# Kernel tuning notes

Hardware: AMD Instinct MI355X
Metric: run time of the kernel (lower is better)

The kernel has to match this reference:

```python
import jax, jax.numpy as jnp
import numpy as np

EMBED = 512
QDIM = 512
VDIM = 512
SRC = 4096
BSZ = 64


def setup_inputs() -> dict:
    key = jax.random.key(0)
    ks = jax.random.split(key, 6)
    query = jax.random.normal(ks[0], (BSZ, QDIM), dtype=jnp.float32)
    value = jax.random.normal(ks[1], (SRC, BSZ, VDIM), dtype=jnp.float32)
    key_padding_mask = jnp.zeros((SRC, BSZ), dtype=bool)
    # params: torch init uniform(-0.1, 0.1); b=0, g=sqrt(1/embed)
    Wq = jax.random.uniform(ks[2], (EMBED, QDIM), minval=-0.1, maxval=0.1, dtype=jnp.float32)
    Wv = jax.random.uniform(ks[3], (EMBED, VDIM), minval=-0.1, maxval=0.1, dtype=jnp.float32)
    v = jax.random.uniform(ks[4], (EMBED,), minval=-0.1, maxval=0.1, dtype=jnp.float32)
    b = jnp.zeros((EMBED,), dtype=jnp.float32)
    g = jnp.full((1,), np.sqrt(1.0 / EMBED), dtype=jnp.float32)
    return {"query": query, "value": value, "key_padding_mask": key_padding_mask,
            "Wq": Wq, "Wv": Wv, "v": v, "b": b, "g": g}


def reference(query, value, key_padding_mask, Wq, Wv, v, b, g):
    # projected_query: [1, bsz, embed]; key: [src, bsz, embed]
    pq = (query @ Wq.T)[None, :, :]
    key = jnp.einsum('sbv,ev->sbe', value, Wv)
    normed_v = g * v / jnp.linalg.norm(v)  # [embed]
    # attn_scores: [src, bsz]
    attn_scores = jnp.einsum('e,sbe->sb', normed_v, jnp.tanh(pq + key + b))
    attn_scores = jnp.where(key_padding_mask, -jnp.inf, attn_scores)
    attn_scores = jax.nn.softmax(attn_scores, axis=0)
    # context: [bsz, value_dim]
    context = jnp.einsum('sb,sbv->bv', attn_scores, value)
    return (context, attn_scores, attn_scores)
```

## Files before the change

### kernel.cpp

```cpp
#include <hip/hip_runtime.h>
#include <hip/hip_bf16.h>
#include <math.h>

typedef __bf16 bf16x8 __attribute__((ext_vector_type(8)));
typedef float  f32x4  __attribute__((ext_vector_type(4)));

#define SRC 4096
#define BSZ 64
#define EMB 512

__global__ void prep_all(const float* __restrict__ query, const float* __restrict__ Wq,
                         const float* __restrict__ bias, const float* __restrict__ v,
                         const float* __restrict__ g, const float* __restrict__ Wv,
                         float* __restrict__ nv, float* __restrict__ pqb,
                         __bf16* __restrict__ wvpk) {
  __shared__ float sh[EMB];
  __shared__ float red[256];
  const int blk = blockIdx.x, t = threadIdx.x;
  if (blk == 0) {
    float a = v[t], b = v[t + 256];
    red[t] = a * a + b * b;
    __syncthreads();
    for (int o = 128; o > 0; o >>= 1) {
      if (t < o) red[t] += red[t + o];
      __syncthreads();
    }
    float scale = g[0] / sqrtf(red[0]);
    nv[t]       = a * scale;
    nv[t + 256] = b * scale;
  } else if (blk <= 128) {
    int tid  = (blk - 1) * 256 + t;
    int lane = tid & 63;
    int ks   = (tid >> 6) & 15;
    int nsub = tid >> 10;
    int e  = nsub * 16 + (lane & 15);
    int k0 = ks * 32 + (lane >> 4) * 8;
    const float* src = Wv + (size_t)e * EMB + k0;
    bf16x8 o;
#pragma unroll
    for (int j = 0; j < 8; ++j) o[j] = (__bf16)src[j];
    *reinterpret_cast<bf16x8*>(wvpk + (size_t)tid * 8) = o;
  } else {
    int bb = blk - 129;
    int b = bb >> 1;
    int e = (bb & 1) * 256 + t;
    sh[t]       = query[b * EMB + t];
    sh[t + 256] = query[b * EMB + t + 256];
    __syncthreads();
    const float* wr = Wq + (size_t)e * EMB;
    float a0 = 0.f, a1 = 0.f;
#pragma unroll 8
    for (int k = 0; k < EMB; k += 8) {
      float4 q0 = *reinterpret_cast<const float4*>(&sh[k]);
      float4 w0 = *reinterpret_cast<const float4*>(&wr[k]);
      float4 q1 = *reinterpret_cast<const float4*>(&sh[k + 4]);
      float4 w1 = *reinterpret_cast<const float4*>(&wr[k + 4]);
      a0 += q0.x * w0.x + q0.y * w0.y + q0.z * w0.z + q0.w * w0.w;
      a1 += q1.x * w1.x + q1.y * w1.y + q1.z * w1.z + q1.w * w1.w;
    }
    pqb[b * EMB + e] = a0 + a1 + bias[e];
  }
}

__global__ __launch_bounds__(512, 4)
void scores_kernel(const float* __restrict__ value, const float* __restrict__ pqb,
                   const float* __restrict__ nv, const __bf16* __restrict__ wvpk,
                   float* __restrict__ scoresT) {
  __shared__ __bf16 As[BSZ * EMB];
  __shared__ float red[8][BSZ];
  const int s = blockIdx.x;
  const int t = threadIdx.x;

  {
    const int row = t >> 3, sub = t & 7;
    const float* src = value + (size_t)s * (BSZ * EMB) + (size_t)row * EMB + sub * 8;
#pragma unroll
    for (int j = 0; j < 8; ++j) {
      float4 v0 = *reinterpret_cast<const float4*>(src + j * 64);
      float4 v1 = *reinterpret_cast<const float4*>(src + j * 64 + 4);
      int kgp = (sub + j * 8) ^ (row & 7);
      bf16x8 o;
      o[0] = (__bf16)v0.x; o[1] = (__bf16)v0.y; o[2] = (__bf16)v0.z; o[3] = (__bf16)v0.w;
      o[4] = (__bf16)v1.x; o[5] = (__bf16)v1.y; o[6] = (__bf16)v1.z; o[7] = (__bf16)v1.w;
      *reinterpret_cast<bf16x8*>(&As[row * EMB + kgp * 8]) = o;
    }
  }
  __syncthreads();

  const int w = t >> 6, l = t & 63, lr = l & 15, lk = l >> 4;

  f32x4 acc[4][4];
#pragma unroll
  for (int m = 0; m < 4; ++m)
#pragma unroll
    for (int n = 0; n < 4; ++n)
#pragma unroll
      for (int r = 0; r < 4; ++r) acc[m][n][r] = 0.f;

  const __bf16* bp = wvpk + (size_t)(w * 4) * 16 * 512 + (size_t)l * 8;
  bf16x8 bq[2][4];
#pragma unroll
  for (int n = 0; n < 4; ++n)
    bq[0][n] = *reinterpret_cast<const bf16x8*>(bp + (size_t)(n * 16) * 512);

#pragma unroll
  for (int ksg = 0; ksg < 16; ++ksg) {
    if (ksg < 15) {
#pragma unroll
      for (int n = 0; n < 4; ++n)
        bq[(ksg + 1) & 1][n] =
            *reinterpret_cast<const bf16x8*>(bp + (size_t)(n * 16 + ksg + 1) * 512);
    }
    const int kgp = ((ksg * 4 + lk) ^ (lr & 7)) * 8;
#pragma unroll
    for (int m = 0; m < 4; ++m) {
      bf16x8 a = *reinterpret_cast<const bf16x8*>(&As[(m * 16 + lr) * EMB + kgp]);
#pragma unroll
      for (int n = 0; n < 4; ++n)
        acc[m][n] = __builtin_amdgcn_mfma_f32_16x16x32_bf16(a, bq[ksg & 1][n], acc[m][n], 0, 0, 0);
    }
  }

  float sc[16];
#pragma unroll
  for (int i = 0; i < 16; ++i) sc[i] = 0.f;
#pragma unroll
  for (int n = 0; n < 4; ++n) {
    int col = w * 64 + n * 16 + lr;
    float nvc = nv[col];
#pragma unroll
    for (int m = 0; m < 4; ++m) {
#pragma unroll
      for (int r = 0; r < 4; ++r) {
        int brow = m * 16 + lk * 4 + r;
        float x = acc[m][n][r] + pqb[brow * EMB + col];
        float e = __expf(2.0f * x);
        float rcp = __builtin_amdgcn_rcpf(1.0f + e);
        sc[m * 4 + r] += fmaf(-2.0f * nvc, rcp, nvc);
      }
    }
  }

#pragma unroll
  for (int i = 0; i < 16; ++i) {
    float vsum = sc[i];
#pragma unroll
    for (int off = 1; off < 16; off <<= 1) vsum += __shfl_xor(vsum, off, 64);
    if (lr == 0) red[w][(i >> 2) * 16 + lk * 4 + (i & 3)] = vsum;
  }
  __syncthreads();
  if (t < BSZ) {
    float total = 0.f;
#pragma unroll
    for (int ww = 0; ww < 8; ++ww) total += red[ww][t];
    scoresT[(size_t)t * SRC + s] = total;
  }
}

__global__ void softmax_k(const float* __restrict__ scoresT, const unsigned char* __restrict__ mask,
                          float* __restrict__ pT, float* __restrict__ attn0,
                          float* __restrict__ attn1) {
  __shared__ float buf[SRC];
  __shared__ float red[256];
  int b = blockIdx.x, t = threadIdx.x;
  float sum = 0.f;
  for (int s = t; s < SRC; s += 256) {
    float x = scoresT[(size_t)b * SRC + s];
    float e = mask[(size_t)s * BSZ + b] ? 0.f : __expf(x);
    buf[s] = e;
    sum += e;
  }
  red[t] = sum; __syncthreads();
  for (int o = 128; o > 0; o >>= 1) { if (t < o) red[t] += red[t + o]; __syncthreads(); }
  float inv = 1.0f / red[0];
  for (int s = t; s < SRC; s += 256) {
    float p = buf[s] * inv;
    pT[(size_t)b * SRC + s] = p;
    attn0[(size_t)s * BSZ + b] = p;
    attn1[(size_t)s * BSZ + b] = p;
  }
}

__global__ __launch_bounds__(256)
void ctx_partial(const float* __restrict__ value, const float* __restrict__ pT,
                 float* __restrict__ parts) {
  int blk = blockIdx.x;
  int c = blk >> 6;
  int b = blk & 63;
  int t = threadIdx.x;
  int f4 = t & 127, half = t >> 7;
  const float* pb = pT + (size_t)b * SRC + c * 256 + half;
  const float* vb = value + ((size_t)(c * 256 + half) * BSZ + b) * EMB + f4 * 4;
  float4 acc = make_float4(0.f, 0.f, 0.f, 0.f);
#pragma unroll 8
  for (int j = 0; j < 128; ++j) {
    float p = pb[j * 2];
    float4 vv = *reinterpret_cast<const float4*>(vb + (size_t)j * 2 * BSZ * EMB);
    acc.x += p * vv.x; acc.y += p * vv.y; acc.z += p * vv.z; acc.w += p * vv.w;
  }
  *reinterpret_cast<float4*>(parts + ((size_t)(c * 2 + half) * BSZ + b) * EMB + f4 * 4) = acc;
}

__global__ void ctx_reduce(const float* __restrict__ parts, float* __restrict__ out_ctx) {
  int idx = blockIdx.x * 256 + threadIdx.x;
  float acc = 0.f;
#pragma unroll
  for (int c = 0; c < 32; ++c) acc += parts[(size_t)c * (BSZ * EMB) + idx];
  out_ctx[idx] = acc;
}

extern "C" void kernel_launch(void* const* d_in, const int* in_sizes, int n_in,
                              void* d_out, int out_size, void* d_ws, size_t ws_size,
                              hipStream_t stream) {
  const float* query        = (const float*)d_in[0];
  const float* value        = (const float*)d_in[1];
  const unsigned char* mask = (const unsigned char*)d_in[2];
  const float* Wq           = (const float*)d_in[3];
  const float* Wv           = (const float*)d_in[4];
  const float* v            = (const float*)d_in[5];
  const float* bias         = (const float*)d_in[6];
  const float* g            = (const float*)d_in[7];

  float* out_ctx = (float*)d_out;
  float* attn0   = (float*)d_out + BSZ * EMB;
  float* attn1   = attn0 + SRC * BSZ;

  char* ws = (char*)d_ws;
  float*  nv      = (float*)(ws);
  float*  pqb     = (float*)(ws + 2048);
  __bf16* wvpk    = (__bf16*)(ws + 2048 + 131072);
  float*  scoresT = (float*)(ws + 2048 + 131072 + 524288);
  float*  pT      = scoresT + SRC * BSZ;
  float*  parts   = pT + SRC * BSZ;

  prep_all<<<257, 256, 0, stream>>>(query, Wq, bias, v, g, Wv, nv, pqb, wvpk);
  scores_kernel<<<SRC, 512, 0, stream>>>(value, pqb, nv, wvpk, scoresT);
  softmax_k<<<BSZ, 256, 0, stream>>>(scoresT, mask, pT, attn0, attn1);
  ctx_partial<<<BSZ * 16, 256, 0, stream>>>(value, pT, parts);
  ctx_reduce<<<128, 256, 0, stream>>>(parts, out_ctx);
}
```

Before: 968.8 us.

## Fuse context accumulation into scores kernel using unnormalized exponentials

The scores kernel now handles 8 source positions per block. Right after computing each score it multiplies the same value slice, still warm in cache, by exp(score) and accumulates per-block partial contexts in registers. The separate ctx_partial pass over the 512MB value tensor and the pT buffer are removed. Softmax now only writes the normaliser Z, and ctx_reduce sums the partials and divides by Z. This relies on the scores being bounded so no max-subtraction is needed. In exchange the grid shrinks to 512 blocks at one block per CU with heavy register use, which lowers occupancy.

Measured after the change: 1.485 ms. 53.3% more time.

```diff
diff --git a/kernel.cpp b/kernel.cpp
--- a/kernel.cpp
+++ b/kernel.cpp
@@ -8,6 +8,7 @@
 #define SRC 4096
 #define BSZ 64
 #define EMB 512
+#define SBLK 8
 
 __global__ void prep_all(const float* __restrict__ query, const float* __restrict__ Wq,
                          const float* __restrict__ bias, const float* __restrict__ v,
@@ -62,103 +63,133 @@
   }
 }
 
-__global__ __launch_bounds__(512, 4)
-void scores_kernel(const float* __restrict__ value, const float* __restrict__ pqb,
-                   const float* __restrict__ nv, const __bf16* __restrict__ wvpk,
-                   float* __restrict__ scoresT) {
+__global__ __launch_bounds__(512, 1)
+void scores_ctx(const float* __restrict__ value, const float* __restrict__ pqb,
+                const float* __restrict__ nv, const __bf16* __restrict__ wvpk,
+                const unsigned char* __restrict__ mask,
+                float* __restrict__ scoresT, float* __restrict__ parts) {
   __shared__ __bf16 As[BSZ * EMB];
   __shared__ float red[8][BSZ];
-  const int s = blockIdx.x;
-  const int t = threadIdx.x;
-
-  {
-    const int row = t >> 3, sub = t & 7;
-    const float* src = value + (size_t)s * (BSZ * EMB) + (size_t)row * EMB + sub * 8;
-#pragma unroll
-    for (int j = 0; j < 8; ++j) {
-      float4 v0 = *reinterpret_cast<const float4*>(src + j * 64);
-      float4 v1 = *reinterpret_cast<const float4*>(src + j * 64 + 4);
-      int kgp = (sub + j * 8) ^ (row & 7);
-      bf16x8 o;
-      o[0] = (__bf16)v0.x; o[1] = (__bf16)v0.y; o[2] = (__bf16)v0.z; o[3] = (__bf16)v0.w;
-      o[4] = (__bf16)v1.x; o[5] = (__bf16)v1.y; o[6] = (__bf16)v1.z; o[7] = (__bf16)v1.w;
-      *reinterpret_cast<bf16x8*>(&As[row * EMB + kgp * 8]) = o;
-    }
-  }
-  __syncthreads();
-
+  __shared__ float esh[BSZ];
+  const int sb = blockIdx.x * SBLK;
+  const int t  = threadIdx.x;
+  const int row = t >> 3, sub = t & 7, swz = row & 7;
   const int w = t >> 6, l = t & 63, lr = l & 15, lk = l >> 4;
-
-  f32x4 acc[4][4];
-#pragma unroll
-  for (int m = 0; m < 4; ++m)
+  const __bf16* bp = wvpk + (size_t)(w * 4) * 16 * 512 + (size_t)l * 8;
+
+  float4 U[16];
+#pragma unroll
+  for (int j = 0; j < 16; ++j) U[j] = make_float4(0.f, 0.f, 0.f, 0.f);
+
+  for (int is = 0; is < SBLK; ++is) {
+    const int s = sb + is;
+
+    {
+      const float* src = value + (size_t)s * (BSZ * EMB) + (size_t)row * EMB + sub * 8;
+#pragma unroll
+      for (int j = 0; j < 8; ++j) {
+        float4 v0 = *reinterpret_cast<const float4*>(src + j * 64);
+        float4 v1 = *reinterpret_cast<const float4*>(src + j * 64 + 4);
+        int kgp = (sub + j * 8) ^ swz;
+        bf16x8 o;
+        o[0] = (__bf16)v0.x; o[1] = (__bf16)v0.y; o[2] = (__bf16)v0.z; o[3] = (__bf16)v0.w;
+        o[4] = (__bf16)v1.x; o[5] = (__bf16)v1.y; o[6] = (__bf16)v1.z; o[7] = (__bf16)v1.w;
+        *reinterpret_cast<bf16x8*>(&As[row * EMB + kgp * 8]) = o;
+      }
+    }
+    __syncthreads();
+
+    f32x4 acc[4][4];
+#pragma unroll
+    for (int m = 0; m < 4; ++m)
+#pragma unroll
+      for (int n = 0; n < 4; ++n)
+#pragma unroll
+        for (int r = 0; r < 4; ++r) acc[m][n][r] = 0.f;
+
+    bf16x8 bq[2][4];
 #pragma unroll
     for (int n = 0; n < 4; ++n)
-#pragma unroll
-      for (int r = 0; r < 4; ++r) acc[m][n][r] = 0.f;
-
-  const __bf16* bp = wvpk + (size_t)(w * 4) * 16 * 512 + (size_t)l * 8;
-  bf16x8 bq[2][4];
-#pragma unroll
-  for (int n = 0; n < 4; ++n)
-    bq[0][n] = *reinterpret_cast<const bf16x8*>(bp + (size_t)(n * 16) * 512);
-
-#pragma unroll
-  for (int ksg = 0; ksg < 16; ++ksg) {
-    if (ksg < 15) {
-#pragma unroll
-      for (int n = 0; n < 4; ++n)
-        bq[(ksg + 1) & 1][n] =
-            *reinterpret_cast<const bf16x8*>(bp + (size_t)(n * 16 + ksg + 1) * 512);
-    }
-    const int kgp = ((ksg * 4 + lk) ^ (lr & 7)) * 8;
-#pragma unroll
-    for (int m = 0; m < 4; ++m) {
-      bf16x8 a = *reinterpret_cast<const bf16x8*>(&As[(m * 16 + lr) * EMB + kgp]);
-#pragma unroll
-      for (int n = 0; n < 4; ++n)
-        acc[m][n] = __builtin_amdgcn_mfma_f32_16x16x32_bf16(a, bq[ksg & 1][n], acc[m][n], 0, 0, 0);
-    }
-  }
-
-  float sc[16];
-#pragma unroll
-  for (int i = 0; i < 16; ++i) sc[i] = 0.f;
-#pragma unroll
-  for (int n = 0; n < 4; ++n) {
-    int col = w * 64 + n * 16 + lr;
-    float nvc = nv[col];
-#pragma unroll
-    for (int m = 0; m < 4; ++m) {
-#pragma unroll
-      for (int r = 0; r < 4; ++r) {
-        int brow = m * 16 + lk * 4 + r;
-        float x = acc[m][n][r] + pqb[brow * EMB + col];
-        float e = __expf(2.0f * x);
-        float rcp = __builtin_amdgcn_rcpf(1.0f + e);
-        sc[m * 4 + r] += fmaf(-2.0f * nvc, rcp, nvc);
-      }
-    }
-  }
-
-#pragma unroll
-  for (int i = 0; i < 16; ++i) {
-    float vsum = sc[i];
-#pragma unroll
-    for (int off = 1; off < 16; off <<= 1) vsum += __shfl_xor(vsum, off, 64);
-    if (lr == 0) red[w][(i >> 2) * 16 + lk * 4 + (i & 3)] = vsum;
-  }
-  __syncthreads();
-  if (t < BSZ) {
-    float total = 0.f;
-#pragma unroll
-    for (int ww = 0; ww < 8; ++ww) total += red[ww][t];
-    scoresT[(size_t)t * SRC + s] = total;
-  }
+      bq[0][n] = *reinterpret_cast<const bf16x8*>(bp + (size_t)(n * 16) * 512);
+
+#pragma unroll
+    for (int ksg = 0; ksg < 16; ++ksg) {
+      if (ksg < 15) {
+#pragma unroll
+        for (int n = 0; n < 4; ++n)
+          bq[(ksg + 1) & 1][n] =
+              *reinterpret_cast<const bf16x8*>(bp + (size_t)(n * 16 + ksg + 1) * 512);
+      }
+      const int kgp = ((ksg * 4 + lk) ^ (lr & 7)) * 8;
+#pragma unroll
+      for (int m = 0; m < 4; ++m) {
+        bf16x8 a = *reinterpret_cast<const bf16x8*>(&As[(m * 16 + lr) * EMB + kgp]);
+#pragma unroll
+        for (int n = 0; n < 4; ++n)
+          acc[m][n] = __builtin_amdgcn_mfma_f32_16x16x32_bf16(a, bq[ksg & 1][n], acc[m][n], 0, 0, 0);
+      }
+    }
+
+    float sc[16];
+#pragma unroll
+    for (int i = 0; i < 16; ++i) sc[i] = 0.f;
+#pragma unroll
+    for (int n = 0; n < 4; ++n) {
+      int col = w * 64 + n * 16 + lr;
+      float nvc = nv[col];
+#pragma unroll
+      for (int m = 0; m < 4; ++m) {
+#pragma unroll
+        for (int r = 0; r < 4; ++r) {
+          int brow = m * 16 + lk * 4 + r;
+          float x = acc[m][n][r] + pqb[brow * EMB + col];
+          float e = __expf(2.0f * x);
+          float rcp = __builtin_amdgcn_rcpf(1.0f + e);
+          sc[m * 4 + r] += fmaf(-2.0f * nvc, rcp, nvc);
+        }
+      }
+    }
+
+#pragma unroll
+    for (int i = 0; i < 16; ++i) {
+      float vsum = sc[i];
+#pragma unroll
+      for (int off = 1; off < 16; off <<= 1) vsum += __shfl_xor(vsum, off, 64);
+      if (lr == 0) red[w][(i >> 2) * 16 + lk * 4 + (i & 3)] = vsum;
+    }
+    __syncthreads();
+
+    if (t < BSZ) {
+      float total = 0.f;
+#pragma unroll
+      for (int ww = 0; ww < 8; ++ww) total += red[ww][t];
+      scoresT[(size_t)t * SRC + s] = total;
+      esh[t] = mask[(size_t)s * BSZ + t] ? 0.f : __expf(total);
+    }
+    __syncthreads();
+
+    {
+      const float* vs = value + (size_t)s * (BSZ * EMB);
+#pragma unroll
+      for (int j = 0; j < 16; ++j) {
+        float eb = esh[j * 4 + (t >> 7)];
+        float4 vv = *reinterpret_cast<const float4*>(vs + (size_t)(j * 512 + t) * 4);
+        U[j].x = fmaf(eb, vv.x, U[j].x);
+        U[j].y = fmaf(eb, vv.y, U[j].y);
+        U[j].z = fmaf(eb, vv.z, U[j].z);
+        U[j].w = fmaf(eb, vv.w, U[j].w);
+      }
+    }
+  }
+
+  float* dst = parts + (size_t)blockIdx.x * (BSZ * EMB);
+#pragma unroll
+  for (int j = 0; j < 16; ++j)
+    *reinterpret_cast<float4*>(dst + (size_t)(j * 512 + t) * 4) = U[j];
 }
 
 __global__ void softmax_k(const float* __restrict__ scoresT, const unsigned char* __restrict__ mask,
-                          float* __restrict__ pT, float* __restrict__ attn0,
+                          float* __restrict__ Z, float* __restrict__ attn0,
                           float* __restrict__ attn1) {
   __shared__ float buf[SRC];
   __shared__ float red[256];
@@ -172,41 +203,44 @@
   }
   red[t] = sum; __syncthreads();
   for (int o = 128; o > 0; o >>= 1) { if (t < o) red[t] += red[t + o]; __syncthreads(); }
+  if (t == 0) Z[b] = red[0];
   float inv = 1.0f / red[0];
   for (int s = t; s < SRC; s += 256) {
     float p = buf[s] * inv;
-    pT[(size_t)b * SRC + s] = p;
     attn0[(size_t)s * BSZ + b] = p;
     attn1[(size_t)s * BSZ + b] = p;
   }
 }
 
 __global__ __launch_bounds__(256)
-void ctx_partial(const float* __restrict__ value, const float* __restrict__ pT,
-                 float* __restrict__ parts) {
-  int blk = blockIdx.x;
-  int c = blk >> 6;
-  int b = blk & 63;
-  int t = threadIdx.x;
-  int f4 = t & 127, half = t >> 7;
-  const float* pb = pT + (size_t)b * SRC + c * 256 + half;
-  const float* vb = value + ((size_t)(c * 256 + half) * BSZ + b) * EMB + f4 * 4;
+void ctx_reduce(const float* __restrict__ parts, const float* __restrict__ Z,
+                float* __restrict__ out_ctx) {
+  __shared__ float4 red4[32][8];
+  const int t = threadIdx.x;
+  const int c = t & 31, jg = t >> 5;
+  const int col = blockIdx.x * 32 + c;
+  const float* src = parts + (size_t)(jg * 64) * (BSZ * EMB) + (size_t)col * 4;
   float4 acc = make_float4(0.f, 0.f, 0.f, 0.f);
 #pragma unroll 8
-  for (int j = 0; j < 128; ++j) {
-    float p = pb[j * 2];
-    float4 vv = *reinterpret_cast<const float4*>(vb + (size_t)j * 2 * BSZ * EMB);
-    acc.x += p * vv.x; acc.y += p * vv.y; acc.z += p * vv.z; acc.w += p * vv.w;
-  }
-  *reinterpret_cast<float4*>(parts + ((size_t)(c * 2 + half) * BSZ + b) * EMB + f4 * 4) = acc;
-}
-
-__global__ void ctx_reduce(const float* __restrict__ parts, float* __restrict__ out_ctx) {
-  int idx = blockIdx.x * 256 + threadIdx.x;
-  float acc = 0.f;
-#pragma unroll
-  for (int c = 0; c < 32; ++c) acc += parts[(size_t)c * (BSZ * EMB) + idx];
-  out_ctx[idx] = acc;
+  for (int j = 0; j < 64; ++j) {
+    float4 vv = *reinterpret_cast<const float4*>(src + (size_t)j * (BSZ * EMB));
+    acc.x += vv.x; acc.y += vv.y; acc.z += vv.z; acc.w += vv.w;
+  }
+  red4[c][jg] = acc;
+  __syncthreads();
+  if (t < 32) {
+    const int cc = t;
+    float4 s0 = red4[cc][0];
+#pragma unroll
+    for (int k = 1; k < 8; ++k) {
+      float4 v = red4[cc][k];
+      s0.x += v.x; s0.y += v.y; s0.z += v.z; s0.w += v.w;
+    }
+    const int colw = blockIdx.x * 32 + cc;
+    const float invz = 1.0f / Z[colw >> 7];
+    s0.x *= invz; s0.y *= invz; s0.z *= invz; s0.w *= invz;
+    *reinterpret_cast<float4*>(out_ctx + (size_t)colw * 4) = s0;
+  }
 }
 
 extern "C" void kernel_launch(void* const* d_in, const int* in_sizes, int n_in,
@@ -228,14 +262,13 @@
   char* ws = (char*)d_ws;
   float*  nv      = (float*)(ws);
   float*  pqb     = (float*)(ws + 2048);
-  __bf16* wvpk    = (__bf16*)(ws + 2048 + 131072);
-  float*  scoresT = (float*)(ws + 2048 + 131072 + 524288);
-  float*  pT      = scoresT + SRC * BSZ;
-  float*  parts   = pT + SRC * BSZ;
+  __bf16* wvpk    = (__bf16*)(ws + 133120);
+  float*  scoresT = (float*)(ws + 657408);
+  float*  Zbuf    = (float*)(ws + 1705984);
+  float*  parts   = (float*)(ws + 1710080);
 
   prep_all<<<257, 256, 0, stream>>>(query, Wq, bias, v, g, Wv, nv, pqb, wvpk);
-  scores_kernel<<<SRC, 512, 0, stream>>>(value, pqb, nv, wvpk, scoresT);
-  softmax_k<<<BSZ, 256, 0, stream>>>(scoresT, mask, pT, attn0, attn1);
-  ctx_partial<<<BSZ * 16, 256, 0, stream>>>(value, pT, parts);
-  ctx_reduce<<<128, 256, 0, stream>>>(parts, out_ctx);
-}
+  scores_ctx<<<SRC / SBLK, 512, 0, stream>>>(value, pqb, nv, wvpk, mask, scoresT, parts);
+  softmax_k<<<BSZ, 256, 0, stream>>>(scoresT, mask, Zbuf, attn0, attn1);
+  ctx_reduce<<<256, 256, 0, stream>>>(parts, Zbuf, out_ctx);
+}
```
